# Kernel tuning notes

Hardware: AMD Instinct MI355X
Metric: run time of the kernel (lower is better)

Reference implementation:

```python
import jax, jax.numpy as jnp
import numpy as np

SENTINEL = 24635
NUM_ENTITIES = 24636
EMB_DIM = 128


def setup_inputs() -> dict:
    key = jax.random.key(0)
    ks = jax.random.split(key, 6)
    B, L = 4096, 50
    return {
        "encoded_context_embs": jax.random.normal(ks[0], (B, 1024), jnp.float32),
        "ent_embs": jax.random.normal(ks[1], (NUM_ENTITIES, EMB_DIM), jnp.float32) * 0.02,
        "W1": jax.random.normal(ks[2], (768, 1024), jnp.float32) * 0.02,
        "W2": jax.random.normal(ks[3], (512, 768), jnp.float32) * 0.02,
        "W3": jax.random.normal(ks[4], (128, 512), jnp.float32) * 0.02,
        "ent_list": jax.random.randint(ks[5], (B, L), 0, NUM_ENTITIES, jnp.int64),
    }


def reference(encoded_context_embs, ent_embs, W1, W2, W3, ent_list):
    # --- ragged gather + masked mean with sentinel early-exit ---
    # valid[b, l] == 1 iff no sentinel appeared at positions <= l (prefix-AND)
    not_sent = (ent_list != SENTINEL).astype(ent_embs.dtype)   # [B, L]
    valid = jnp.cumprod(not_sent, axis=1)                      # [B, L]
    gathered = ent_embs[ent_list]                              # [B, L, D]
    cnt = valid.sum(axis=1)                                    # [B]
    summed = jnp.einsum("bl,bld->bd", valid, gathered)        # [B, D]
    mean = summed / jnp.maximum(cnt, 1.0)[:, None]
    # sentinel at position 0 -> fall back to the sentinel embedding
    user_embs = jnp.where((cnt == 0)[:, None], ent_embs[SENTINEL][None, :], mean)

    # --- MLP on pooled context: 1024 -> 768 -> 512 -> 128 ---
    x = jax.nn.relu(encoded_context_embs @ W1.T)
    x = jax.nn.relu(x @ W2.T)
    q = x @ W3.T                                               # [B, 128]

    # --- cross attention: query=q, key=value=user_embs ---
    scale = 1.0 / jnp.sqrt(jnp.asarray(q.shape[-1], q.dtype))
    scores = (q @ user_embs.T) * scale                         # [B, B]
    weights = jax.nn.softmax(scores, axis=-1)
    return weights @ user_embs                                 # [B, 128]
```

## Files before the change

kernel.cpp:

```cpp
#include <hip/hip_runtime.h>
#include <hip/hip_bf16.h>

#define SENTINEL 24635

typedef unsigned char f8_t;
using bf16x8  = __attribute__((ext_vector_type(8))) __bf16;
using bf16x2  = __attribute__((ext_vector_type(2))) __bf16;
using floatx4 = __attribute__((ext_vector_type(4))) float;

__device__ inline bf16x8 cvt8(float4 a, float4 b) {
  bf16x8 v;
  v[0] = (__bf16)a.x; v[1] = (__bf16)a.y; v[2] = (__bf16)a.z; v[3] = (__bf16)a.w;
  v[4] = (__bf16)b.x; v[5] = (__bf16)b.y; v[6] = (__bf16)b.z; v[7] = (__bf16)b.w;
  return v;
}

__device__ inline void store_fp8x8(f8_t* d, float4 a, float4 b, float s) {
  int w0 = __builtin_amdgcn_cvt_pk_fp8_f32(a.x * s, a.y * s, 0, false);
  w0 = __builtin_amdgcn_cvt_pk_fp8_f32(a.z * s, a.w * s, w0, true);
  int w1 = __builtin_amdgcn_cvt_pk_fp8_f32(b.x * s, b.y * s, 0, false);
  w1 = __builtin_amdgcn_cvt_pk_fp8_f32(b.z * s, b.w * s, w1, true);
  int2 v; v.x = w0; v.y = w1;
  *(int2*)d = v;
}

__device__ inline void gll16(const void* g, void* l) {
  __builtin_amdgcn_global_load_lds(
      (const __attribute__((address_space(1))) unsigned int*)g,
      (__attribute__((address_space(3))) unsigned int*)l, 16, 0, 0);
}

__global__ __launch_bounds__(256) void prep_kernel(
    const float* __restrict__ s0, f8_t* __restrict__ d0,
    const float* __restrict__ s1, f8_t* __restrict__ d1,
    const float* __restrict__ s2, f8_t* __restrict__ d2,
    const float* __restrict__ s3, f8_t* __restrict__ d3,
    const float* __restrict__ ent, const int* __restrict__ ent_list,
    __bf16* __restrict__ user_n) {
  if (blockIdx.x < 2656) {
    int g = blockIdx.x * 256 + threadIdx.x;
    const float* s; f8_t* d; int i; float sc;
    if (g < 524288)      { s = s0; d = d0; i = g;          sc = 1.f;  }
    else if (g < 622592) { s = s1; d = d1; i = g - 524288; sc = 16.f; }
    else if (g < 671744) { s = s2; d = d2; i = g - 622592; sc = 16.f; }
    else if (g < 679936) { s = s3; d = d3; i = g - 671744; sc = 16.f; }
    else return;
    i *= 8;
    float4 a = *(const float4*)(s + i);
    float4 b = *(const float4*)(s + i + 4);
    store_fp8x8(d + i, a, b, sc);
    return;
  }
  const int b = (blockIdx.x - 2656) * 4 + (threadIdx.x >> 6);
  const int lane = threadIdx.x & 63;
  int myidx = (lane < 50) ? ent_list[b * 50 + lane] : 0;
  unsigned long long m = __ballot(lane < 50 && myidx == SENTINEL);
  const int cnt = (m == 0) ? 50 : (int)__builtin_ctzll(m);

  float sx = 0.f, sy = 0.f;
  for (int l0 = 0; l0 < 50; l0 += 10) {
    if (l0 >= cnt) break;
    float2 e[10];
#pragma unroll
    for (int j = 0; j < 10; ++j) {
      int idx = __shfl(myidx, l0 + j);
      e[j] = *(const float2*)(ent + (size_t)idx * 128 + lane * 2);
    }
#pragma unroll
    for (int j = 0; j < 10; ++j) {
      if (l0 + j < cnt) { sx += e[j].x; sy += e[j].y; }
    }
  }
  float vx, vy;
  if (cnt == 0) {
    float2 e = *(const float2*)(ent + (size_t)SENTINEL * 128 + lane * 2);
    vx = e.x; vy = e.y;
  } else {
    float inv = 1.f / (float)cnt;
    vx = sx * inv; vy = sy * inv;
  }
  bf16x2 o; o[0] = (__bf16)vx; o[1] = (__bf16)vy;
  *(bf16x2*)(user_n + (size_t)b * 128 + lane * 2) = o;
}

template <int WR, int WC, int MT, int NT, int RELU, bool OUT_BF16>
__device__ inline void gemm_body_f8(const f8_t* __restrict__ A,
                                    const f8_t* __restrict__ W,
                                    void* __restrict__ Cout,
                                    int M, int N, int K, int bn0, int bm0,
                                    char* lds) {
  constexpr int BM = WR * MT * 16;
  constexpr int BN = WC * NT * 16;
  auto As = (f8_t (*)[BM][32])lds;
  auto Bs = (f8_t (*)[BN][32])(lds + (size_t)2 * BM * 32);
  const int tid  = threadIdx.x;
  const int w    = tid >> 6;
  const int lane = tid & 63;
  const int quad = lane >> 4;
  const int l16  = lane & 15;
  const int wr   = w / WC;
  const int wc   = w % WC;
  const int lrow = lane >> 1;
  const int lcol = (lane & 1) * 16;

  floatx4 acc[MT][NT];
#pragma unroll
  for (int mt = 0; mt < MT; ++mt)
#pragma unroll
    for (int nt = 0; nt < NT; ++nt) acc[mt][nt] = (floatx4){0.f, 0.f, 0.f, 0.f};

  constexpr int nAc = 2 * (BM / 32);
  constexpr int nBc = 2 * (BN / 32);
  for (int k0 = 0; k0 < K; k0 += 64) {
    __syncthreads();
#pragma unroll
    for (int c = w; c < nAc; c += 4) {
      int s = c / (BM / 32);
      int r = (c % (BM / 32)) * 32;
      gll16(A + (size_t)(bm0 + r + lrow) * K + k0 + s * 32 + lcol, &As[s][r][0]);
    }
#pragma unroll
    for (int c = w; c < nBc; c += 4) {
      int s = c / (BN / 32);
      int r = (c % (BN / 32)) * 32;
      gll16(W + (size_t)(bn0 + r + lrow) * K + k0 + s * 32 + lcol, &Bs[s][r][0]);
    }
    __syncthreads();
#pragma unroll
    for (int s = 0; s < 2; ++s) {
      long af[MT], bfr[NT];
#pragma unroll
      for (int mt = 0; mt < MT; ++mt)
        af[mt] = *(const long*)&As[s][wr * (MT * 16) + mt * 16 + l16][quad * 8];
#pragma unroll
      for (int nt = 0; nt < NT; ++nt)
        bfr[nt] = *(const long*)&Bs[s][wc * (NT * 16) + nt * 16 + l16][quad * 8];
#pragma unroll
      for (int mt = 0; mt < MT; ++mt)
#pragma unroll
        for (int nt = 0; nt < NT; ++nt)
          acc[mt][nt] = __builtin_amdgcn_mfma_f32_16x16x32_fp8_fp8(
              af[mt], bfr[nt], acc[mt][nt], 0, 0, 0);
    }
  }

  const float osc = 0.0625f;
#pragma unroll
  for (int mt = 0; mt < MT; ++mt) {
    const int row0 = bm0 + wr * (MT * 16) + mt * 16 + quad * 4;
#pragma unroll
    for (int nt = 0; nt < NT; ++nt) {
      const int col = bn0 + wc * (NT * 16) + nt * 16 + l16;
#pragma unroll
      for (int r = 0; r < 4; ++r) {
        float v = acc[mt][nt][r] * osc;
        if (RELU) v = fmaxf(v, 0.f);
        if (OUT_BF16) {
          ((__bf16*)Cout)[(size_t)(row0 + r) * N + col] = (__bf16)v;
        } else {
          int p = __builtin_amdgcn_cvt_pk_fp8_f32(v, v, 0, false);
          ((f8_t*)Cout)[(size_t)(row0 + r) * N + col] = (f8_t)(p & 0xff);
        }
      }
    }
  }
}

template <int WR, int WC, int MT, int NT, int RELU, bool OUT_BF16>
__global__ __launch_bounds__(256) void gemm_f8(const f8_t* __restrict__ A,
                                               const f8_t* __restrict__ W,
                                               void* __restrict__ C,
                                               int M, int N, int K) {
  __shared__ char lds[(size_t)2 * ((WR * MT * 16) + (WC * NT * 16)) * 32];
  gemm_body_f8<WR, WC, MT, NT, RELU, OUT_BF16>(
      A, W, C, M, N, K, blockIdx.x * (WC * NT * 16), blockIdx.y * (WR * MT * 16),
      lds);
}

__global__ __launch_bounds__(256) void gemm1_tr(const f8_t* __restrict__ A,
                                                const f8_t* __restrict__ W,
                                                f8_t* __restrict__ C,
                                                const __bf16* __restrict__ un,
                                                __bf16* __restrict__ ut) {
  __shared__ char lds[10240];
  const int bx = blockIdx.x;
  if (bx < 512) {
    gemm_body_f8<2, 2, 2, 3, 1, false>(A, W, C, 4096, 768, 1024,
                                       (bx % 8) * 96, (bx / 8) * 64, lds);
    return;
  }
  const int idx = bx - 512;
  const int r0 = (idx & 63) * 64;
  const int c0 = (idx >> 6) * 64;
  auto T = (__bf16 (*)[72])lds;
  const int tid = threadIdx.x;
#pragma unroll
  for (int p = 0; p < 2; ++p) {
    int r = (tid >> 3) + p * 32;
    int c = (tid & 7) * 8;
    *(bf16x8*)&T[r][c] = *(const bf16x8*)(un + (size_t)(r0 + r) * 128 + c0 + c);
  }
  __syncthreads();
#pragma unroll
  for (int p = 0; p < 2; ++p) {
    int c = (tid >> 3) + p * 32;
    int r = (tid & 7) * 8;
    bf16x8 v;
#pragma unroll
    for (int j = 0; j < 8; ++j) v[j] = T[r + j][c];
    *(bf16x8*)(ut + (size_t)(c0 + c) * 4096 + r0 + r) = v;
  }
}

__global__ __launch_bounds__(256) void flash_attn(const __bf16* __restrict__ Q,
                                                  const __bf16* __restrict__ Un_g,
                                                  const __bf16* __restrict__ Ut_g,
                                                  __bf16* __restrict__ O_part,
                                                  float* __restrict__ lp) {
  __shared__ __bf16 Un[64][136];
  __shared__ __bf16 Ut[128][72];
  __shared__ __bf16 Ps[4][32][72];
  const int tid  = threadIdx.x;
  const int w    = tid >> 6;
  const int lane = tid & 63;
  const int quad = lane >> 4;
  const int l16  = lane & 15;
  const int qrow0 = blockIdx.x * 128;
  const int split = blockIdx.y;
  const float scale = 0.08838834764831845f;

  bf16x8 aq[2][4];
#pragma unroll
  for (int mt = 0; mt < 2; ++mt)
#pragma unroll
    for (int c = 0; c < 4; ++c)
      aq[mt][c] = *(const bf16x8*)(Q + (size_t)(qrow0 + w * 32 + mt * 16 + l16) * 128 +
                                   c * 32 + quad * 8);

  floatx4 o[2][8];
#pragma unroll
  for (int mt = 0; mt < 2; ++mt)
#pragma unroll
    for (int t = 0; t < 8; ++t) o[mt][t] = (floatx4){0.f, 0.f, 0.f, 0.f};
  float lsum[2][4] = {{0.f, 0.f, 0.f, 0.f}, {0.f, 0.f, 0.f, 0.f}};

  for (int chunk = 0; chunk < 4; ++chunk) {
    const int key0 = (split * 4 + chunk) * 64;
    __syncthreads();
#pragma unroll
    for (int p = 0; p < 4; ++p) {
      int r = (tid >> 4) + p * 16;
      int c = (tid & 15) * 8;
      *(bf16x8*)&Un[r][c] = *(const bf16x8*)(Un_g + (size_t)(key0 + r) * 128 + c);
    }
#pragma unroll
    for (int p = 0; p < 4; ++p) {
      int d = (tid >> 3) + p * 32;
      int kk = (tid & 7) * 8;
      *(bf16x8*)&Ut[d][kk] = *(const bf16x8*)(Ut_g + (size_t)d * 4096 + key0 + kk);
    }
    __syncthreads();

#pragma unroll
    for (int t = 0; t < 4; ++t) {
      bf16x8 bk[4];
#pragma unroll
      for (int c = 0; c < 4; ++c)
        bk[c] = *(const bf16x8*)&Un[t * 16 + l16][c * 32 + quad * 8];
      floatx4 s0 = (floatx4){0.f, 0.f, 0.f, 0.f};
      floatx4 s1 = (floatx4){0.f, 0.f, 0.f, 0.f};
#pragma unroll
      for (int c = 0; c < 4; ++c) {
        s0 = __builtin_amdgcn_mfma_f32_16x16x32_bf16(aq[0][c], bk[c], s0, 0, 0, 0);
        s1 = __builtin_amdgcn_mfma_f32_16x16x32_bf16(aq[1][c], bk[c], s1, 0, 0, 0);
      }
#pragma unroll
      for (int r = 0; r < 4; ++r) {
        float p0 = __expf(s0[r] * scale);
        float p1 = __expf(s1[r] * scale);
        lsum[0][r] += p0;
        lsum[1][r] += p1;
        Ps[w][quad * 4 + r][t * 16 + l16] = (__bf16)p0;
        Ps[w][16 + quad * 4 + r][t * 16 + l16] = (__bf16)p1;
      }
    }

#pragma unroll
    for (int c2 = 0; c2 < 2; ++c2) {
      bf16x8 ap0 = *(const bf16x8*)&Ps[w][l16][c2 * 32 + quad * 8];
      bf16x8 ap1 = *(const bf16x8*)&Ps[w][16 + l16][c2 * 32 + quad * 8];
#pragma unroll
      for (int dt = 0; dt < 8; ++dt) {
        bf16x8 bv = *(const bf16x8*)&Ut[dt * 16 + l16][c2 * 32 + quad * 8];
        o[0][dt] = __builtin_amdgcn_mfma_f32_16x16x32_bf16(ap0, bv, o[0][dt], 0, 0, 0);
        o[1][dt] = __builtin_amdgcn_mfma_f32_16x16x32_bf16(ap1, bv, o[1][dt], 0, 0, 0);
      }
    }
  }

#pragma unroll
  for (int mt = 0; mt < 2; ++mt)
#pragma unroll
    for (int r = 0; r < 4; ++r) {
      float v = lsum[mt][r];
      v += __shfl_xor(v, 1);
      v += __shfl_xor(v, 2);
      v += __shfl_xor(v, 4);
      v += __shfl_xor(v, 8);
      lsum[mt][r] = v;
    }

  __bf16* Ob = O_part + (size_t)split * 524288;
#pragma unroll
  for (int mt = 0; mt < 2; ++mt) {
    const int row0 = qrow0 + w * 32 + mt * 16 + quad * 4;
#pragma unroll
    for (int dt = 0; dt < 8; ++dt) {
#pragma unroll
      for (int r = 0; r < 4; ++r) {
        Ob[(size_t)(row0 + r) * 128 + dt * 16 + l16] = (__bf16)o[mt][dt][r];
      }
    }
    if (l16 == 0) {
#pragma unroll
      for (int r = 0; r < 4; ++r) lp[(size_t)split * 4096 + row0 + r] = lsum[mt][r];
    }
  }
}

__global__ __launch_bounds__(256) void combine_kernel(const __bf16* __restrict__ Op,
                                                      const float* __restrict__ lp,
                                                      float* __restrict__ out) {
  const int i = (blockIdx.x * 256 + threadIdx.x) * 8;
  const int row = i >> 7;
  float num[8] = {0.f, 0.f, 0.f, 0.f, 0.f, 0.f, 0.f, 0.f};
  float den = 0.f;
#pragma unroll
  for (int s = 0; s < 16; ++s) {
    bf16x8 v = *(const bf16x8*)(Op + (size_t)s * 524288 + i);
#pragma unroll
    for (int j = 0; j < 8; ++j) num[j] += (float)v[j];
    den += lp[(size_t)s * 4096 + row];
  }
  float inv = 1.f / den;
  float4 r0 = {num[0] * inv, num[1] * inv, num[2] * inv, num[3] * inv};
  float4 r1 = {num[4] * inv, num[5] * inv, num[6] * inv, num[7] * inv};
  *(float4*)(out + i) = r0;
  *(float4*)(out + i + 4) = r1;
}

extern "C" void kernel_launch(void* const* d_in, const int* in_sizes, int n_in,
                              void* d_out, int out_size, void* d_ws, size_t ws_size,
                              hipStream_t stream) {
  (void)in_sizes; (void)n_in; (void)out_size; (void)ws_size;
  const float* ctx      = (const float*)d_in[0];
  const float* ent_embs = (const float*)d_in[1];
  const float* W1       = (const float*)d_in[2];
  const float* W2       = (const float*)d_in[3];
  const float* W3       = (const float*)d_in[4];
  const int*   ent_list = (const int*)d_in[5];
  float* out = (float*)d_out;

  char* base = (char*)d_ws;
  __bf16* user_n = (__bf16*)(base);
  __bf16* user_t = (__bf16*)(base + (1ull << 20));
  __bf16* qb     = (__bf16*)(base + (2ull << 20));
  float*  lp     = (float*)(base + (3ull << 20));
  f8_t*   ctxb   = (f8_t*)(base + (4ull << 20));
  f8_t*   W1b    = (f8_t*)(base + (8ull << 20));
  f8_t*   W2b    = (f8_t*)(base + 9175040ull);
  f8_t*   W3b    = (f8_t*)(base + 9568256ull);
  f8_t*   x1b    = (f8_t*)(base + (10ull << 20));
  f8_t*   x2b    = (f8_t*)(base + (13ull << 20));
  __bf16* O_part = (__bf16*)(base + (15ull << 20));

  prep_kernel<<<3680, 256, 0, stream>>>(ctx, ctxb, W1, W1b, W2, W2b, W3, W3b,
                                        ent_embs, ent_list, user_n);
  gemm1_tr<<<640, 256, 0, stream>>>(ctxb, W1b, x1b, user_n, user_t);
  gemm_f8<2, 2, 2, 2, 1, false><<<dim3(8, 64), 256, 0, stream>>>(
      x1b, W2b, x2b, 4096, 512, 768);
  gemm_f8<2, 2, 1, 2, 0, true><<<dim3(2, 128), 256, 0, stream>>>(
      x2b, W3b, qb, 4096, 128, 512);
  flash_attn<<<dim3(32, 16), 256, 0, stream>>>(qb, user_n, user_t, O_part, lp);
  combine_kernel<<<256, 256, 0, stream>>>(O_part, lp, out);
}
```

Measured before the change: 155.6 us.

## Fuse context fp8 conversion into GEMM1 and combine into flash attention

The separate fp8 conversion of the 4096x1024 context matrix in the prep kernel is removed. GEMM1 now loads fp32 context directly, converts to fp8 in registers and stores to LDS, replacing the async global-to-LDS load. The standalone combine kernel is replaced by a last-block-done atomic counter per query tile, so the final split-K reduction happens inside flash_attn. Both changes save a kernel launch and an intermediate round trip, at the cost of synchronous fp32 loads in GEMM1 (read roughly 8x redundantly across N tiles) and an added memset.

```diff
diff --git a/kernel.cpp b/kernel.cpp
--- a/kernel.cpp
+++ b/kernel.cpp
@@ -15,12 +15,13 @@
   return v;
 }
 
+__device__ inline int pack4_fp8(float4 a, float s) {
+  int w = __builtin_amdgcn_cvt_pk_fp8_f32(a.x * s, a.y * s, 0, false);
+  return __builtin_amdgcn_cvt_pk_fp8_f32(a.z * s, a.w * s, w, true);
+}
+
 __device__ inline void store_fp8x8(f8_t* d, float4 a, float4 b, float s) {
-  int w0 = __builtin_amdgcn_cvt_pk_fp8_f32(a.x * s, a.y * s, 0, false);
-  w0 = __builtin_amdgcn_cvt_pk_fp8_f32(a.z * s, a.w * s, w0, true);
-  int w1 = __builtin_amdgcn_cvt_pk_fp8_f32(b.x * s, b.y * s, 0, false);
-  w1 = __builtin_amdgcn_cvt_pk_fp8_f32(b.z * s, b.w * s, w1, true);
-  int2 v; v.x = w0; v.y = w1;
+  int2 v; v.x = pack4_fp8(a, s); v.y = pack4_fp8(b, s);
   *(int2*)d = v;
 }
 
@@ -31,27 +32,25 @@
 }
 
 __global__ __launch_bounds__(256) void prep_kernel(
-    const float* __restrict__ s0, f8_t* __restrict__ d0,
     const float* __restrict__ s1, f8_t* __restrict__ d1,
     const float* __restrict__ s2, f8_t* __restrict__ d2,
     const float* __restrict__ s3, f8_t* __restrict__ d3,
     const float* __restrict__ ent, const int* __restrict__ ent_list,
     __bf16* __restrict__ user_n) {
-  if (blockIdx.x < 2656) {
+  if (blockIdx.x < 608) {
     int g = blockIdx.x * 256 + threadIdx.x;
-    const float* s; f8_t* d; int i; float sc;
-    if (g < 524288)      { s = s0; d = d0; i = g;          sc = 1.f;  }
-    else if (g < 622592) { s = s1; d = d1; i = g - 524288; sc = 16.f; }
-    else if (g < 671744) { s = s2; d = d2; i = g - 622592; sc = 16.f; }
-    else if (g < 679936) { s = s3; d = d3; i = g - 671744; sc = 16.f; }
+    const float* s; f8_t* d; int i;
+    if (g < 98304)       { s = s1; d = d1; i = g; }
+    else if (g < 147456) { s = s2; d = d2; i = g - 98304; }
+    else if (g < 155648) { s = s3; d = d3; i = g - 147456; }
     else return;
     i *= 8;
     float4 a = *(const float4*)(s + i);
     float4 b = *(const float4*)(s + i + 4);
-    store_fp8x8(d + i, a, b, sc);
+    store_fp8x8(d + i, a, b, 16.f);
     return;
   }
-  const int b = (blockIdx.x - 2656) * 4 + (threadIdx.x >> 6);
+  const int b = (blockIdx.x - 608) * 4 + (threadIdx.x >> 6);
   const int lane = threadIdx.x & 63;
   int myidx = (lane < 50) ? ent_list[b * 50 + lane] : 0;
   unsigned long long m = __ballot(lane < 50 && myidx == SENTINEL);
@@ -83,8 +82,8 @@
   *(bf16x2*)(user_n + (size_t)b * 128 + lane * 2) = o;
 }
 
-template <int WR, int WC, int MT, int NT, int RELU, bool OUT_BF16>
-__device__ inline void gemm_body_f8(const f8_t* __restrict__ A,
+template <int WR, int WC, int MT, int NT, int RELU, bool OUT_BF16, bool A_F32>
+__device__ inline void gemm_body_f8(const void* __restrict__ Aptr,
                                     const f8_t* __restrict__ W,
                                     void* __restrict__ Cout,
                                     int M, int N, int K, int bn0, int bm0,
@@ -117,7 +116,21 @@
     for (int c = w; c < nAc; c += 4) {
       int s = c / (BM / 32);
       int r = (c % (BM / 32)) * 32;
-      gll16(A + (size_t)(bm0 + r + lrow) * K + k0 + s * 32 + lcol, &As[s][r][0]);
+      if constexpr (A_F32) {
+        const float* ap = (const float*)Aptr +
+                          (size_t)(bm0 + r + lrow) * K + k0 + s * 32 + lcol;
+        float4 a0 = *(const float4*)ap;
+        float4 a1 = *(const float4*)(ap + 4);
+        float4 a2 = *(const float4*)(ap + 8);
+        float4 a3 = *(const float4*)(ap + 12);
+        int4 pk;
+        pk.x = pack4_fp8(a0, 1.f); pk.y = pack4_fp8(a1, 1.f);
+        pk.z = pack4_fp8(a2, 1.f); pk.w = pack4_fp8(a3, 1.f);
+        *(int4*)&As[s][r + lrow][lcol] = pk;
+      } else {
+        gll16((const f8_t*)Aptr + (size_t)(bm0 + r + lrow) * K + k0 + s * 32 + lcol,
+              &As[s][r][0]);
+      }
     }
 #pragma unroll
     for (int c = w; c < nBc; c += 4) {
@@ -172,12 +185,12 @@
                                                void* __restrict__ C,
                                                int M, int N, int K) {
   __shared__ char lds[(size_t)2 * ((WR * MT * 16) + (WC * NT * 16)) * 32];
-  gemm_body_f8<WR, WC, MT, NT, RELU, OUT_BF16>(
+  gemm_body_f8<WR, WC, MT, NT, RELU, OUT_BF16, false>(
       A, W, C, M, N, K, blockIdx.x * (WC * NT * 16), blockIdx.y * (WR * MT * 16),
       lds);
 }
 
-__global__ __launch_bounds__(256) void gemm1_tr(const f8_t* __restrict__ A,
+__global__ __launch_bounds__(256) void gemm1_tr(const float* __restrict__ A,
                                                 const f8_t* __restrict__ W,
                                                 f8_t* __restrict__ C,
                                                 const __bf16* __restrict__ un,
@@ -185,8 +198,8 @@
   __shared__ char lds[10240];
   const int bx = blockIdx.x;
   if (bx < 512) {
-    gemm_body_f8<2, 2, 2, 3, 1, false>(A, W, C, 4096, 768, 1024,
-                                       (bx % 8) * 96, (bx / 8) * 64, lds);
+    gemm_body_f8<2, 2, 2, 3, 1, false, true>(A, W, C, 4096, 768, 1024,
+                                             (bx % 8) * 96, (bx / 8) * 64, lds);
     return;
   }
   const int idx = bx - 512;
@@ -216,7 +229,9 @@
                                                   const __bf16* __restrict__ Un_g,
                                                   const __bf16* __restrict__ Ut_g,
                                                   __bf16* __restrict__ O_part,
-                                                  float* __restrict__ lp) {
+                                                  float* __restrict__ lp,
+                                                  unsigned* __restrict__ done,
+                                                  float* __restrict__ out) {
   __shared__ __bf16 Un[64][136];
   __shared__ __bf16 Ut[128][72];
   __shared__ __bf16 Ps[4][32][72];
@@ -225,7 +240,8 @@
   const int lane = tid & 63;
   const int quad = lane >> 4;
   const int l16  = lane & 15;
-  const int qrow0 = blockIdx.x * 128;
+  const int qtile = blockIdx.x;
+  const int qrow0 = qtile * 128;
   const int split = blockIdx.y;
   const float scale = 0.08838834764831845f;
 
@@ -326,27 +342,40 @@
       for (int r = 0; r < 4; ++r) lp[(size_t)split * 4096 + row0 + r] = lsum[mt][r];
     }
   }
-}
-
-__global__ __launch_bounds__(256) void combine_kernel(const __bf16* __restrict__ Op,
-                                                      const float* __restrict__ lp,
-                                                      float* __restrict__ out) {
-  const int i = (blockIdx.x * 256 + threadIdx.x) * 8;
-  const int row = i >> 7;
-  float num[8] = {0.f, 0.f, 0.f, 0.f, 0.f, 0.f, 0.f, 0.f};
-  float den = 0.f;
-#pragma unroll
-  for (int s = 0; s < 16; ++s) {
-    bf16x8 v = *(const bf16x8*)(Op + (size_t)s * 524288 + i);
-#pragma unroll
-    for (int j = 0; j < 8; ++j) num[j] += (float)v[j];
-    den += lp[(size_t)s * 4096 + row];
-  }
-  float inv = 1.f / den;
-  float4 r0 = {num[0] * inv, num[1] * inv, num[2] * inv, num[3] * inv};
-  float4 r1 = {num[4] * inv, num[5] * inv, num[6] * inv, num[7] * inv};
-  *(float4*)(out + i) = r0;
-  *(float4*)(out + i + 4) = r1;
+
+  __syncthreads();
+  int* flagp = (int*)&Un[0][0];
+  if (tid == 0) {
+    __threadfence();
+    unsigned old = __hip_atomic_fetch_add(done + qtile, 1u, __ATOMIC_ACQ_REL,
+                                          __HIP_MEMORY_SCOPE_AGENT);
+    __threadfence();
+    *flagp = (old == 15u) ? 1 : 0;
+  }
+  __syncthreads();
+  if (*flagp) {
+    const int row = qrow0 + (tid >> 1);
+    const int col0 = (tid & 1) * 64;
+    float den = 0.f;
+#pragma unroll
+    for (int s = 0; s < 16; ++s) den += lp[(size_t)s * 4096 + row];
+    const float inv = 1.f / den;
+#pragma unroll
+    for (int c8 = 0; c8 < 8; ++c8) {
+      float num[8] = {0.f, 0.f, 0.f, 0.f, 0.f, 0.f, 0.f, 0.f};
+#pragma unroll
+      for (int s = 0; s < 16; ++s) {
+        bf16x8 v = *(const bf16x8*)(O_part + (size_t)s * 524288 +
+                                    (size_t)row * 128 + col0 + c8 * 8);
+#pragma unroll
+        for (int j = 0; j < 8; ++j) num[j] += (float)v[j];
+      }
+      float4 r0 = {num[0] * inv, num[1] * inv, num[2] * inv, num[3] * inv};
+      float4 r1 = {num[4] * inv, num[5] * inv, num[6] * inv, num[7] * inv};
+      *(float4*)(out + (size_t)row * 128 + col0 + c8 * 8) = r0;
+      *(float4*)(out + (size_t)row * 128 + col0 + c8 * 8 + 4) = r1;
+    }
+  }
 }
 
 extern "C" void kernel_launch(void* const* d_in, const int* in_sizes, int n_in,
@@ -366,21 +395,23 @@
   __bf16* user_t = (__bf16*)(base + (1ull << 20));
   __bf16* qb     = (__bf16*)(base + (2ull << 20));
   float*  lp     = (float*)(base + (3ull << 20));
-  f8_t*   ctxb   = (f8_t*)(base + (4ull << 20));
-  f8_t*   W1b    = (f8_t*)(base + (8ull << 20));
-  f8_t*   W2b    = (f8_t*)(base + 9175040ull);
-  f8_t*   W3b    = (f8_t*)(base + 9568256ull);
-  f8_t*   x1b    = (f8_t*)(base + (10ull << 20));
-  f8_t*   x2b    = (f8_t*)(base + (13ull << 20));
-  __bf16* O_part = (__bf16*)(base + (15ull << 20));
-
-  prep_kernel<<<3680, 256, 0, stream>>>(ctx, ctxb, W1, W1b, W2, W2b, W3, W3b,
+  f8_t*   W1b    = (f8_t*)(base + (4ull << 20));
+  f8_t*   W2b    = (f8_t*)(base + 5242880ull);
+  f8_t*   W3b    = (f8_t*)(base + 5636096ull);
+  f8_t*   x1b    = (f8_t*)(base + (6ull << 20));
+  f8_t*   x2b    = (f8_t*)(base + (9ull << 20));
+  __bf16* O_part = (__bf16*)(base + (11ull << 20));
+  unsigned* done = (unsigned*)(base + (240ull << 20));
+
+  hipMemsetAsync(done, 0, 128, stream);
+
+  prep_kernel<<<1632, 256, 0, stream>>>(W1, W1b, W2, W2b, W3, W3b,
                                         ent_embs, ent_list, user_n);
-  gemm1_tr<<<640, 256, 0, stream>>>(ctxb, W1b, x1b, user_n, user_t);
+  gemm1_tr<<<640, 256, 0, stream>>>(ctx, W1b, x1b, user_n, user_t);
   gemm_f8<2, 2, 2, 2, 1, false><<<dim3(8, 64), 256, 0, stream>>>(
       x1b, W2b, x2b, 4096, 512, 768);
   gemm_f8<2, 2, 1, 2, 0, true><<<dim3(2, 128), 256, 0, stream>>>(
       x2b, W3b, qb, 4096, 128, 512);
-  flash_attn<<<dim3(32, 16), 256, 0, stream>>>(qb, user_n, user_t, O_part, lp);
-  combine_kernel<<<256, 256, 0, stream>>>(O_part, lp, out);
-}
+  flash_attn<<<dim3(32, 16), 256, 0, stream>>>(qb, user_n, user_t, O_part, lp,
+                                               done, out);
+}
```

After: 227.3 us. 1.46x slower.
